# Kernel optimization log

Hardware: AMD Instinct MI355X
Metric: run time of the kernel (lower is better)

Reference implementation:

```python
import jax, jax.numpy as jnp
import numpy as np

EPS = 1e-6

def elu_feature_map(x):
    return jax.nn.elu(x) + 1.0

def setup_inputs() -> dict:
    key = jax.random.key(0)
    k1, k2, k3 = jax.random.split(key, 3)
    N, S, H, D, M = 16, 4096, 16, 64, 64
    query = jax.random.normal(k1, (N, H, D), dtype=jnp.float32)
    keys = jax.random.normal(k2, (N, S, H, D), dtype=jnp.float32)
    values = jax.random.normal(k3, (N, S, H, M), dtype=jnp.float32)
    key_mask = jnp.ones((N, S), dtype=jnp.float32)  # key_lengths.float_matrix
    return {"query": query, "keys": keys, "values": values, "key_mask": key_mask}

def reference(query, keys, values, key_mask):
    # Q: [N,H,D]
    Q = elu_feature_map(query)
    # K: [N,S,H,D], masked over sequence
    K = elu_feature_map(keys) * key_mask[:, :, None, None]
    # S_state: [N,H,M,D] -- K^T V outer-product reduction over sequence
    S_state = jnp.einsum('nshd,nshm->nhmd', K, values)
    # Z: [N,H,D] -- normalizer
    Z = K.sum(axis=1)
    # QZ: [N,H]
    QZ = 1.0 / (jnp.einsum('nhd,nhd->nh', Q, Z) + EPS)
    # V_out: [N,H,M]
    V_out = jnp.einsum('nhd,nhmd,nh->nhm', Q, S_state, QZ)
    return (V_out, S_state, Z)
```

## Files before the change

### kernel.cpp

```cpp
#include <hip/hip_runtime.h>


#define S_LEN  4096
#define NHEAD  16
#define DDIM   64
#define MDIM   64
#define NWAVE  4
#define CH_S   32
#define PITCH  1024
#define WS_ROW 4160

#define OUT_SOFF  (16 * 16 * 64)
#define OUT_ZOFF  (OUT_SOFF + 16 * 16 * 64 * 64)

using short8 = __attribute__((ext_vector_type(8))) short;
using f32x4  = __attribute__((ext_vector_type(4))) float;
using uint4v = __attribute__((ext_vector_type(4))) unsigned int;

union FragCast { uint4v u; short8 s; };

__device__ __forceinline__ float elup1(float x) {
    return x > 0.0f ? x + 1.0f : __expf(x);
}

__device__ __forceinline__ unsigned bfpack(float a, float b) {
    union { float f; unsigned u; } ca, cb;
    ca.f = a; cb.f = b;
    const unsigned ra = ca.u + 0x7FFFu + ((ca.u >> 16) & 1u);
    const unsigned rb = cb.u + 0x7FFFu + ((cb.u >> 16) & 1u);
    return (ra >> 16) | (rb & 0xFFFF0000u);
}

__device__ __forceinline__ const float* rfl_ptr(const float* p) {
    unsigned long long u = (unsigned long long)p;
    const unsigned lo = __builtin_amdgcn_readfirstlane((unsigned)u);
    const unsigned hi = __builtin_amdgcn_readfirstlane((unsigned)(u >> 32));
    return (const float*)(((unsigned long long)hi << 32) | lo);
}

__global__ __launch_bounds__(256, 1)
void rcla_partial(const float* __restrict__ keys,
                  const float* __restrict__ values,
                  const float* __restrict__ kmask,
                  float* __restrict__ ws,
                  int nchk, int psh)
{
    __shared__ float mbuf[64][68];

    const int t    = threadIdx.x;
    const int wave = t >> 6;
    const int lane = t & 63;
    const int c16  = lane & 15;
    const int g    = lane >> 4;
    const int part = blockIdx.x & ((1 << psh) - 1);
    const int pair = blockIdx.x >> psh;
    const int nIdx = pair >> 4;
    const int hIdx = pair & 15;

    const int sWave = part * (S_LEN >> psh) + wave * (nchk * CH_S);
    const size_t base = ((size_t)nIdx * S_LEN + sWave) * PITCH
                      + (size_t)hIdx * DDIM;
    const float* kbase = rfl_ptr(keys   + base) ;
    const float* vbase = rfl_ptr(values + base);
    const float* mbase = rfl_ptr(kmask + (size_t)nIdx * S_LEN + sWave);

    f32x4 acc[4][4];
#pragma unroll
    for (int i = 0; i < 4; ++i)
#pragma unroll
        for (int j = 0; j < 4; ++j) acc[i][j] = f32x4{0.f, 0.f, 0.f, 0.f};
    float zz[4] = {0.f, 0.f, 0.f, 0.f};

    for (int ch = 0; ch < nchk; ++ch) {
        const int s0 = ch * CH_S + g * 8;

        float kraw[4][8];
#pragma unroll
        for (int j = 0; j < 8; ++j) {
            const size_t ro = (size_t)(s0 + j) * PITCH + c16;
#pragma unroll
            for (int tj = 0; tj < 4; ++tj)
                kraw[tj][j] = kbase[ro + tj * 16];
        }
        float mk[8];
#pragma unroll
        for (int j = 0; j < 8; ++j) mk[j] = mbase[s0 + j];

        float vraw[4][8];
#pragma unroll
        for (int j = 0; j < 8; ++j) {
            const size_t ro = (size_t)(s0 + j) * PITCH + c16;
#pragma unroll
            for (int ti = 0; ti < 4; ++ti)
                vraw[ti][j] = vbase[ro + ti * 16];
        }

        unsigned kf[4][4], vf[4][4];
#pragma unroll
        for (int tj = 0; tj < 4; ++tj)
#pragma unroll
            for (int q = 0; q < 4; ++q) {
                const float e0 = elup1(kraw[tj][2 * q])     * mk[2 * q];
                const float e1 = elup1(kraw[tj][2 * q + 1]) * mk[2 * q + 1];
                zz[tj] += e0 + e1;
                kf[tj][q] = bfpack(e0, e1);
            }
#pragma unroll
        for (int ti = 0; ti < 4; ++ti)
#pragma unroll
            for (int q = 0; q < 4; ++q)
                vf[ti][q] = bfpack(vraw[ti][2 * q], vraw[ti][2 * q + 1]);

#pragma unroll
        for (int ti = 0; ti < 4; ++ti) {
            FragCast fa;
            fa.u = uint4v{vf[ti][0], vf[ti][1], vf[ti][2], vf[ti][3]};
#pragma unroll
            for (int tj = 0; tj < 4; ++tj) {
                FragCast fb;
                fb.u = uint4v{kf[tj][0], kf[tj][1], kf[tj][2], kf[tj][3]};
                acc[ti][tj] = __builtin_amdgcn_mfma_f32_16x16x32_bf16(
                    fa.s, fb.s, acc[ti][tj], 0, 0, 0);
            }
        }
    }

#pragma unroll
    for (int tj = 0; tj < 4; ++tj) {
        zz[tj] += __shfl_xor(zz[tj], 16, 64);
        zz[tj] += __shfl_xor(zz[tj], 32, 64);
    }

    __syncthreads();

    for (int rr = 0; rr < 4; ++rr) {
        if (wave == rr) {
#pragma unroll
            for (int ti = 0; ti < 4; ++ti)
#pragma unroll
                for (int tj = 0; tj < 4; ++tj)
#pragma unroll
                    for (int r = 0; r < 4; ++r) {
                        const int m = ti * 16 + g * 4 + r;
                        const int d = tj * 16 + c16;
                        if (rr == 0) mbuf[m][d]  = acc[ti][tj][r];
                        else         mbuf[m][d] += acc[ti][tj][r];
                    }
        }
        __syncthreads();
    }

    float* wrow = ws + (size_t)blockIdx.x * WS_ROW;
    {
        const int m  = t >> 2;
        const int dc = (t & 3) * 16;
#pragma unroll
        for (int j = 0; j < 16; j += 4)
            *(float4*)&wrow[m * 64 + dc + j] = *(const float4*)&mbuf[m][dc + j];
    }
    __syncthreads();

    if (g == 0) {
#pragma unroll
        for (int tj = 0; tj < 4; ++tj)
            mbuf[wave][tj * 16 + c16] = zz[tj];
    }
    __syncthreads();
    if (t < 64) {
        float zv = 0.f;
#pragma unroll
        for (int r = 0; r < NWAVE; ++r) zv += mbuf[r][t];
        wrow[64 * 64 + t] = zv;
    }
}

__global__ __launch_bounds__(256)
void rcla_reduce(const float* __restrict__ query,
                 const float* __restrict__ ws,
                 float* __restrict__ out,
                 int nsplit)
{
    __shared__ float S[64][68];
    __shared__ float zb[64];
    __shared__ float qb[64];

    const int p = blockIdx.x;
    const int t = threadIdx.x;
    const float* bp = ws + (size_t)p * nsplit * WS_ROW;

    const int m  = t >> 2;
    const int dc = (t & 3) * 16;
    float4 a[4];
#pragma unroll
    for (int j = 0; j < 4; ++j) a[j] = make_float4(0.f, 0.f, 0.f, 0.f);
    for (int part = 0; part < nsplit; ++part) {
        const float* w = bp + (size_t)part * WS_ROW + m * 64 + dc;
#pragma unroll
        for (int j = 0; j < 4; ++j) {
            const float4 x = *(const float4*)&w[j * 4];
            a[j].x += x.x; a[j].y += x.y; a[j].z += x.z; a[j].w += x.w;
        }
    }
#pragma unroll
    for (int j = 0; j < 4; ++j) {
        *(float4*)&out[OUT_SOFF + (size_t)p * 4096 + m * 64 + dc + j * 4] = a[j];
        *(float4*)&S[m][dc + j * 4] = a[j];
    }
    if (t < 64) {
        float zv = 0.f;
        for (int part = 0; part < nsplit; ++part)
            zv += bp[(size_t)part * WS_ROW + 64 * 64 + t];
        out[OUT_ZOFF + (size_t)p * 64 + t] = zv;
        zb[t] = zv;
        qb[t] = elup1(query[(size_t)p * 64 + t]);
    }
    __syncthreads();

    if (t < 64) {
        float zp = qb[t] * zb[t];
#pragma unroll
        for (int off = 32; off >= 1; off >>= 1) zp += __shfl_xor(zp, off, 64);
        const float qz = 1.0f / (zp + 1e-6f);
        float vs = 0.0f;
#pragma unroll
        for (int d = 0; d < 64; d += 4) {
            const float4 sv = *(const float4*)&S[t][d];
            vs = fmaf(qb[d],     sv.x, vs);
            vs = fmaf(qb[d + 1], sv.y, vs);
            vs = fmaf(qb[d + 2], sv.z, vs);
            vs = fmaf(qb[d + 3], sv.w, vs);
        }
        out[(size_t)p * 64 + t] = qz * vs;
    }
}

extern "C" void kernel_launch(void* const* d_in, const int* in_sizes, int n_in,
                              void* d_out, int out_size, void* d_ws, size_t ws_size,
                              hipStream_t stream) {
    const float* q  = (const float*)d_in[0];
    const float* k  = (const float*)d_in[1];
    const float* v  = (const float*)d_in[2];
    const float* km = (const float*)d_in[3];
    float* out = (float*)d_out;
    float* wsf = (float*)d_ws;

    int psh = 2;
    if (ws_size < (size_t)256 * 4 * WS_ROW * sizeof(float)) psh = 1;
    if (ws_size < (size_t)256 * 2 * WS_ROW * sizeof(float)) psh = 0;
    const int split = 1 << psh;
    const int nchk  = (S_LEN >> psh) / (NWAVE * CH_S);

    rcla_partial<<<dim3(256 * split), dim3(256), 0, stream>>>(k, v, km, wsf, nchk, psh);
    rcla_reduce <<<dim3(256),         dim3(256), 0, stream>>>(q, wsf, out, split);
}
```

Baseline: 124.1 us.

## Fuse partial and reduce kernels with double-buffered global-to-LDS async loads

Merges the split partial kernel and the reduce kernel into one kernel with one block per (n,h) pair, which removes the workspace round trip and the second launch. Keys, values and mask are streamed into a per-wave double-buffered LDS area with global_load_lds, gated by vmcnt waits, so memory fetch overlaps the MFMA compute of the previous chunk. The trade-off is only 256 blocks of 4 waves each and no sequence split, so there may be too little parallelism to saturate HBM on a 256-CU part. Correctness relies on the hand-counted vmcnt values matching the 17 loads issued per chunk.

```diff
diff --git a/kernel.cpp b/kernel.cpp
--- a/kernel.cpp
+++ b/kernel.cpp
@@ -7,8 +7,8 @@
 #define MDIM   64
 #define NWAVE  4
 #define CH_S   32
+#define NCHK   32
 #define PITCH  1024
-#define WS_ROW 4160
 
 #define OUT_SOFF  (16 * 16 * 64)
 #define OUT_ZOFF  (OUT_SOFF + 16 * 16 * 64 * 64)
@@ -18,6 +18,18 @@
 using uint4v = __attribute__((ext_vector_type(4))) unsigned int;
 
 union FragCast { uint4v u; short8 s; };
+
+typedef const __attribute__((address_space(1))) void gvoid_t;
+typedef __attribute__((address_space(3))) void lvoid_t;
+
+#define GLOAD16(dst, src) \
+    __builtin_amdgcn_global_load_lds((gvoid_t*)(src), (lvoid_t*)(dst), 16, 0, 0)
+#define GLOAD4(dst, src) \
+    __builtin_amdgcn_global_load_lds((gvoid_t*)(src), (lvoid_t*)(dst), 4, 0, 0)
+#define WAITVM17 do { asm volatile("s_waitcnt vmcnt(17)" ::: "memory"); \
+                      __builtin_amdgcn_sched_barrier(0); } while (0)
+#define WAITVM0  do { asm volatile("s_waitcnt vmcnt(0)"  ::: "memory"); \
+                      __builtin_amdgcn_sched_barrier(0); } while (0)
 
 __device__ __forceinline__ float elup1(float x) {
     return x > 0.0f ? x + 1.0f : __expf(x);
@@ -31,38 +43,42 @@
     return (ra >> 16) | (rb & 0xFFFF0000u);
 }
 
-__device__ __forceinline__ const float* rfl_ptr(const float* p) {
-    unsigned long long u = (unsigned long long)p;
-    const unsigned lo = __builtin_amdgcn_readfirstlane((unsigned)u);
-    const unsigned hi = __builtin_amdgcn_readfirstlane((unsigned)(u >> 32));
-    return (const float*)(((unsigned long long)hi << 32) | lo);
-}
+struct WaveBuf {
+    float K[CH_S][DDIM];
+    float V[CH_S][MDIM];
+    float mk[64];
+};
 
 __global__ __launch_bounds__(256, 1)
-void rcla_partial(const float* __restrict__ keys,
-                  const float* __restrict__ values,
-                  const float* __restrict__ kmask,
-                  float* __restrict__ ws,
-                  int nchk, int psh)
+void rcla_fused(const float* __restrict__ query,
+                const float* __restrict__ keys,
+                const float* __restrict__ values,
+                const float* __restrict__ kmask,
+                float* __restrict__ out)
 {
+    __shared__ WaveBuf hot[NWAVE][2];
     __shared__ float mbuf[64][68];
+    __shared__ float zrows[NWAVE][64];
+    __shared__ float qb[64];
+    __shared__ float zb[64];
 
     const int t    = threadIdx.x;
     const int wave = t >> 6;
     const int lane = t & 63;
     const int c16  = lane & 15;
     const int g    = lane >> 4;
-    const int part = blockIdx.x & ((1 << psh) - 1);
-    const int pair = blockIdx.x >> psh;
+    const int pair = blockIdx.x;
     const int nIdx = pair >> 4;
     const int hIdx = pair & 15;
 
-    const int sWave = part * (S_LEN >> psh) + wave * (nchk * CH_S);
+    const int sWave = wave * (NCHK * CH_S);
     const size_t base = ((size_t)nIdx * S_LEN + sWave) * PITCH
                       + (size_t)hIdx * DDIM;
-    const float* kbase = rfl_ptr(keys   + base) ;
-    const float* vbase = rfl_ptr(values + base);
-    const float* mbase = rfl_ptr(kmask + (size_t)nIdx * S_LEN + sWave);
+    const int li = lane >> 4;
+    const int ci = lane & 15;
+    const float* kl = keys   + base + (size_t)li * PITCH + ci * 4;
+    const float* vl = values + base + (size_t)li * PITCH + ci * 4;
+    const float* ml = kmask + (size_t)nIdx * S_LEN + sWave + (lane & 31);
 
     f32x4 acc[4][4];
 #pragma unroll
@@ -71,37 +87,43 @@
         for (int j = 0; j < 4; ++j) acc[i][j] = f32x4{0.f, 0.f, 0.f, 0.f};
     float zz[4] = {0.f, 0.f, 0.f, 0.f};
 
-    for (int ch = 0; ch < nchk; ++ch) {
-        const int s0 = ch * CH_S + g * 8;
-
-        float kraw[4][8];
-#pragma unroll
-        for (int j = 0; j < 8; ++j) {
-            const size_t ro = (size_t)(s0 + j) * PITCH + c16;
-#pragma unroll
-            for (int tj = 0; tj < 4; ++tj)
-                kraw[tj][j] = kbase[ro + tj * 16];
-        }
-        float mk[8];
-#pragma unroll
-        for (int j = 0; j < 8; ++j) mk[j] = mbase[s0 + j];
-
-        float vraw[4][8];
-#pragma unroll
-        for (int j = 0; j < 8; ++j) {
-            const size_t ro = (size_t)(s0 + j) * PITCH + c16;
-#pragma unroll
-            for (int ti = 0; ti < 4; ++ti)
-                vraw[ti][j] = vbase[ro + ti * 16];
-        }
+    auto issue = [&](int p, int ch) {
+        const size_t co = (size_t)ch * CH_S * PITCH;
+        float* Kd = &hot[wave][p].K[0][0];
+        float* Vd = &hot[wave][p].V[0][0];
+#pragma unroll
+        for (int r = 0; r < 8; ++r)
+            GLOAD16(Kd + r * 256, kl + co + (size_t)r * 4 * PITCH);
+#pragma unroll
+        for (int r = 0; r < 8; ++r)
+            GLOAD16(Vd + r * 256, vl + co + (size_t)r * 4 * PITCH);
+        GLOAD4(&hot[wave][p].mk[0], ml + ch * CH_S);
+    };
+
+    auto compute = [&](int p) {
+        const WaveBuf& B = hot[wave][p];
+        float mk8[8];
+#pragma unroll
+        for (int j = 0; j < 8; ++j) mk8[j] = B.mk[g * 8 + j];
+        float kraw[4][8], vraw[4][8];
+#pragma unroll
+        for (int tj = 0; tj < 4; ++tj)
+#pragma unroll
+            for (int j = 0; j < 8; ++j)
+                kraw[tj][j] = B.K[g * 8 + j][tj * 16 + c16];
+#pragma unroll
+        for (int ti = 0; ti < 4; ++ti)
+#pragma unroll
+            for (int j = 0; j < 8; ++j)
+                vraw[ti][j] = B.V[g * 8 + j][ti * 16 + c16];
 
         unsigned kf[4][4], vf[4][4];
 #pragma unroll
         for (int tj = 0; tj < 4; ++tj)
 #pragma unroll
             for (int q = 0; q < 4; ++q) {
-                const float e0 = elup1(kraw[tj][2 * q])     * mk[2 * q];
-                const float e1 = elup1(kraw[tj][2 * q + 1]) * mk[2 * q + 1];
+                const float e0 = elup1(kraw[tj][2 * q])     * mk8[2 * q];
+                const float e1 = elup1(kraw[tj][2 * q + 1]) * mk8[2 * q + 1];
                 zz[tj] += e0 + e1;
                 kf[tj][q] = bfpack(e0, e1);
             }
@@ -123,7 +145,23 @@
                     fa.s, fb.s, acc[ti][tj], 0, 0, 0);
             }
         }
-    }
+    };
+
+    issue(0, 0);
+#pragma unroll 1
+    for (int c = 0; c < NCHK - 2; c += 2) {
+        issue(1, c + 1);
+        WAITVM17;
+        compute(0);
+        issue(0, c + 2);
+        WAITVM17;
+        compute(1);
+    }
+    issue(1, NCHK - 1);
+    WAITVM17;
+    compute(0);
+    WAITVM0;
+    compute(1);
 
 #pragma unroll
     for (int tj = 0; tj < 4; ++tj) {
@@ -150,87 +188,45 @@
         __syncthreads();
     }
 
-    float* wrow = ws + (size_t)blockIdx.x * WS_ROW;
+    if (g == 0) {
+#pragma unroll
+        for (int tj = 0; tj < 4; ++tj)
+            zrows[wave][tj * 16 + c16] = zz[tj];
+    }
+    if (t < 64) qb[t] = elup1(query[(size_t)pair * DDIM + t]);
+
     {
         const int m  = t >> 2;
         const int dc = (t & 3) * 16;
 #pragma unroll
         for (int j = 0; j < 16; j += 4)
-            *(float4*)&wrow[m * 64 + dc + j] = *(const float4*)&mbuf[m][dc + j];
+            *(float4*)&out[OUT_SOFF + (size_t)pair * 4096 + m * 64 + dc + j] =
+                *(const float4*)&mbuf[m][dc + j];
     }
     __syncthreads();
 
-    if (g == 0) {
-#pragma unroll
-        for (int tj = 0; tj < 4; ++tj)
-            mbuf[wave][tj * 16 + c16] = zz[tj];
+    if (t < 64) {
+        const float zv = zrows[0][t] + zrows[1][t] + zrows[2][t] + zrows[3][t];
+        out[OUT_ZOFF + (size_t)pair * 64 + t] = zv;
+        zb[t] = zv;
     }
     __syncthreads();
-    if (t < 64) {
-        float zv = 0.f;
-#pragma unroll
-        for (int r = 0; r < NWAVE; ++r) zv += mbuf[r][t];
-        wrow[64 * 64 + t] = zv;
-    }
-}
-
-__global__ __launch_bounds__(256)
-void rcla_reduce(const float* __restrict__ query,
-                 const float* __restrict__ ws,
-                 float* __restrict__ out,
-                 int nsplit)
-{
-    __shared__ float S[64][68];
-    __shared__ float zb[64];
-    __shared__ float qb[64];
-
-    const int p = blockIdx.x;
-    const int t = threadIdx.x;
-    const float* bp = ws + (size_t)p * nsplit * WS_ROW;
-
-    const int m  = t >> 2;
-    const int dc = (t & 3) * 16;
-    float4 a[4];
-#pragma unroll
-    for (int j = 0; j < 4; ++j) a[j] = make_float4(0.f, 0.f, 0.f, 0.f);
-    for (int part = 0; part < nsplit; ++part) {
-        const float* w = bp + (size_t)part * WS_ROW + m * 64 + dc;
-#pragma unroll
-        for (int j = 0; j < 4; ++j) {
-            const float4 x = *(const float4*)&w[j * 4];
-            a[j].x += x.x; a[j].y += x.y; a[j].z += x.z; a[j].w += x.w;
-        }
-    }
-#pragma unroll
-    for (int j = 0; j < 4; ++j) {
-        *(float4*)&out[OUT_SOFF + (size_t)p * 4096 + m * 64 + dc + j * 4] = a[j];
-        *(float4*)&S[m][dc + j * 4] = a[j];
-    }
-    if (t < 64) {
-        float zv = 0.f;
-        for (int part = 0; part < nsplit; ++part)
-            zv += bp[(size_t)part * WS_ROW + 64 * 64 + t];
-        out[OUT_ZOFF + (size_t)p * 64 + t] = zv;
-        zb[t] = zv;
-        qb[t] = elup1(query[(size_t)p * 64 + t]);
-    }
-    __syncthreads();
-
-    if (t < 64) {
-        float zp = qb[t] * zb[t];
+
+    if (wave == 0) {
+        float zp = qb[lane] * zb[lane];
 #pragma unroll
         for (int off = 32; off >= 1; off >>= 1) zp += __shfl_xor(zp, off, 64);
         const float qz = 1.0f / (zp + 1e-6f);
         float vs = 0.0f;
 #pragma unroll
         for (int d = 0; d < 64; d += 4) {
-            const float4 sv = *(const float4*)&S[t][d];
+            const float4 sv = *(const float4*)&mbuf[lane][d];
             vs = fmaf(qb[d],     sv.x, vs);
             vs = fmaf(qb[d + 1], sv.y, vs);
             vs = fmaf(qb[d + 2], sv.z, vs);
             vs = fmaf(qb[d + 3], sv.w, vs);
         }
-        out[(size_t)p * 64 + t] = qz * vs;
+        out[(size_t)pair * MDIM + lane] = qz * vs;
     }
 }
 
@@ -242,14 +238,5 @@
     const float* v  = (const float*)d_in[2];
     const float* km = (const float*)d_in[3];
     float* out = (float*)d_out;
-    float* wsf = (float*)d_ws;
-
-    int psh = 2;
-    if (ws_size < (size_t)256 * 4 * WS_ROW * sizeof(float)) psh = 1;
-    if (ws_size < (size_t)256 * 2 * WS_ROW * sizeof(float)) psh = 0;
-    const int split = 1 << psh;
-    const int nchk  = (S_LEN >> psh) / (NWAVE * CH_S);
-
-    rcla_partial<<<dim3(256 * split), dim3(256), 0, stream>>>(k, v, km, wsf, nchk, psh);
-    rcla_reduce <<<dim3(256),         dim3(256), 0, stream>>>(q, wsf, out, split);
-}
+    rcla_fused<<<dim3(256), dim3(256), 0, stream>>>(q, k, v, km, out);
+}
```

Measured after the change: 106.3 us. -14.4%, faster.

## Stream K/V through LDS via async global_load_lds with 4-stage per-wave pipeline

Applied to the files above, without the earlier changes.

Replaces direct per-lane global loads of keys and values with asynchronous global_load_lds copies into a 4-deep per-wave LDS ring, using explicit vmcnt waits so loads for upcoming chunks overlap with transform and MFMA work on the current one. The split across sequence parts is removed: each block now covers one (n,h) pair and each wave writes its own partial S and Z row straight to workspace, which the reduce kernel sums, dropping the LDS cross-wave reduction and its barriers. Half the lanes transform each 16-row chunk alternately, and MFMAs fire every two chunks. The grid shrinks to 256 blocks with large LDS use, which may lower occupancy and memory-level parallelism, and the fixed workspace size no longer falls back when ws_size is small.

```diff
diff --git a/kernel.cpp b/kernel.cpp
--- a/kernel.cpp
+++ b/kernel.cpp
@@ -6,7 +6,8 @@
 #define DDIM   64
 #define MDIM   64
 #define NWAVE  4
-#define CH_S   32
+#define CH_S   16
+#define NCHK   64
 #define PITCH  1024
 #define WS_ROW 4160
 
@@ -18,6 +19,16 @@
 using uint4v = __attribute__((ext_vector_type(4))) unsigned int;
 
 union FragCast { uint4v u; short8 s; };
+
+typedef const __attribute__((address_space(1))) void gvoid_t;
+typedef __attribute__((address_space(3))) void lvoid_t;
+
+#define GLOAD16(dst, src) \
+    __builtin_amdgcn_global_load_lds((gvoid_t*)(src), (lvoid_t*)(dst), 16, 0, 0)
+#define GLOAD4(dst, src) \
+    __builtin_amdgcn_global_load_lds((gvoid_t*)(src), (lvoid_t*)(dst), 4, 0, 0)
+#define WAITVM(N) do { asm volatile("s_waitcnt vmcnt(" #N ")" ::: "memory"); \
+                       __builtin_amdgcn_sched_barrier(0); } while (0)
 
 __device__ __forceinline__ float elup1(float x) {
     return x > 0.0f ? x + 1.0f : __expf(x);
@@ -31,38 +42,34 @@
     return (ra >> 16) | (rb & 0xFFFF0000u);
 }
 
-__device__ __forceinline__ const float* rfl_ptr(const float* p) {
-    unsigned long long u = (unsigned long long)p;
-    const unsigned lo = __builtin_amdgcn_readfirstlane((unsigned)u);
-    const unsigned hi = __builtin_amdgcn_readfirstlane((unsigned)(u >> 32));
-    return (const float*)(((unsigned long long)hi << 32) | lo);
-}
-
 __global__ __launch_bounds__(256, 1)
 void rcla_partial(const float* __restrict__ keys,
                   const float* __restrict__ values,
                   const float* __restrict__ kmask,
-                  float* __restrict__ ws,
-                  int nchk, int psh)
+                  float* __restrict__ ws)
 {
-    __shared__ float mbuf[64][68];
+    __shared__ float Kbuf[NWAVE][4][CH_S * DDIM];
+    __shared__ float Vbuf[NWAVE][4][CH_S * DDIM];
+    __shared__ float maskL[NWAVE][1024];
 
     const int t    = threadIdx.x;
     const int wave = t >> 6;
     const int lane = t & 63;
     const int c16  = lane & 15;
     const int g    = lane >> 4;
-    const int part = blockIdx.x & ((1 << psh) - 1);
-    const int pair = blockIdx.x >> psh;
+    const int pair = blockIdx.x;
     const int nIdx = pair >> 4;
     const int hIdx = pair & 15;
 
-    const int sWave = part * (S_LEN >> psh) + wave * (nchk * CH_S);
+    const int sWave = wave * (NCHK * CH_S);
     const size_t base = ((size_t)nIdx * S_LEN + sWave) * PITCH
                       + (size_t)hIdx * DDIM;
-    const float* kbase = rfl_ptr(keys   + base) ;
-    const float* vbase = rfl_ptr(values + base);
-    const float* mbase = rfl_ptr(kmask + (size_t)nIdx * S_LEN + sWave);
+    const int li = lane >> 4;
+    const int ci = lane & 15;
+    const float* kl = keys   + base + (size_t)li * PITCH + ci * 4;
+    const float* vl = values + base + (size_t)li * PITCH + ci * 4;
+    const float* msrc = kmask + (size_t)nIdx * S_LEN + sWave + lane;
+    float* maskb = &maskL[wave][0];
 
     f32x4 acc[4][4];
 #pragma unroll
@@ -70,47 +77,56 @@
 #pragma unroll
         for (int j = 0; j < 4; ++j) acc[i][j] = f32x4{0.f, 0.f, 0.f, 0.f};
     float zz[4] = {0.f, 0.f, 0.f, 0.f};
-
-    for (int ch = 0; ch < nchk; ++ch) {
-        const int s0 = ch * CH_S + g * 8;
-
-        float kraw[4][8];
-#pragma unroll
-        for (int j = 0; j < 8; ++j) {
-            const size_t ro = (size_t)(s0 + j) * PITCH + c16;
+    unsigned kf[4][4], vf[4][4];
+
+    auto issue = [&](int b, int ch) {
+        const size_t co = (size_t)ch * CH_S * PITCH;
+        float* Kd = &Kbuf[wave][0][0] + b * (CH_S * DDIM);
+        float* Vd = &Vbuf[wave][0][0] + b * (CH_S * DDIM);
+#pragma unroll
+        for (int r = 0; r < 4; ++r)
+            GLOAD16(Kd + r * 256, kl + co + (size_t)r * 4 * PITCH);
+#pragma unroll
+        for (int r = 0; r < 4; ++r)
+            GLOAD16(Vd + r * 256, vl + co + (size_t)r * 4 * PITCH);
+    };
+
+    auto xform = [&](int b, int ch, int par) {
+        if ((g >> 1) == par) {
+            const int r0 = (g & 1) * 8;
+            const float* Kb = &Kbuf[wave][0][0] + b * (CH_S * DDIM);
+            const float* Vb = &Vbuf[wave][0][0] + b * (CH_S * DDIM);
+            float mk8[8], kraw[4][8], vraw[4][8];
+#pragma unroll
+            for (int j = 0; j < 8; ++j) mk8[j] = maskb[ch * CH_S + r0 + j];
 #pragma unroll
             for (int tj = 0; tj < 4; ++tj)
-                kraw[tj][j] = kbase[ro + tj * 16];
-        }
-        float mk[8];
-#pragma unroll
-        for (int j = 0; j < 8; ++j) mk[j] = mbase[s0 + j];
-
-        float vraw[4][8];
-#pragma unroll
-        for (int j = 0; j < 8; ++j) {
-            const size_t ro = (size_t)(s0 + j) * PITCH + c16;
+#pragma unroll
+                for (int j = 0; j < 8; ++j)
+                    kraw[tj][j] = Kb[(r0 + j) * DDIM + tj * 16 + c16];
 #pragma unroll
             for (int ti = 0; ti < 4; ++ti)
-                vraw[ti][j] = vbase[ro + ti * 16];
-        }
-
-        unsigned kf[4][4], vf[4][4];
-#pragma unroll
-        for (int tj = 0; tj < 4; ++tj)
-#pragma unroll
-            for (int q = 0; q < 4; ++q) {
-                const float e0 = elup1(kraw[tj][2 * q])     * mk[2 * q];
-                const float e1 = elup1(kraw[tj][2 * q + 1]) * mk[2 * q + 1];
-                zz[tj] += e0 + e1;
-                kf[tj][q] = bfpack(e0, e1);
-            }
-#pragma unroll
-        for (int ti = 0; ti < 4; ++ti)
-#pragma unroll
-            for (int q = 0; q < 4; ++q)
-                vf[ti][q] = bfpack(vraw[ti][2 * q], vraw[ti][2 * q + 1]);
-
+#pragma unroll
+                for (int j = 0; j < 8; ++j)
+                    vraw[ti][j] = Vb[(r0 + j) * DDIM + ti * 16 + c16];
+#pragma unroll
+            for (int tj = 0; tj < 4; ++tj)
+#pragma unroll
+                for (int q = 0; q < 4; ++q) {
+                    const float e0 = elup1(kraw[tj][2 * q])     * mk8[2 * q];
+                    const float e1 = elup1(kraw[tj][2 * q + 1]) * mk8[2 * q + 1];
+                    zz[tj] += e0 + e1;
+                    kf[tj][q] = bfpack(e0, e1);
+                }
+#pragma unroll
+            for (int ti = 0; ti < 4; ++ti)
+#pragma unroll
+                for (int q = 0; q < 4; ++q)
+                    vf[ti][q] = bfpack(vraw[ti][2 * q], vraw[ti][2 * q + 1]);
+        }
+    };
+
+    auto domfma = [&]() {
 #pragma unroll
         for (int ti = 0; ti < 4; ++ti) {
             FragCast fa;
@@ -123,7 +139,27 @@
                     fa.s, fb.s, acc[ti][tj], 0, 0, 0);
             }
         }
-    }
+    };
+
+#pragma unroll
+    for (int grp = 0; grp < 16; ++grp)
+        GLOAD4(maskb + grp * 64, msrc + grp * 64);
+    issue(0, 0);
+    issue(1, 1);
+    issue(2, 2);
+
+#pragma unroll 1
+    for (int tt = 0; tt < 15; ++tt) {
+        const int c0 = 4 * tt;
+        WAITVM(16); issue(3, c0 + 3); xform(0, c0 + 0, 0);
+        WAITVM(16); issue(0, c0 + 4); xform(1, c0 + 1, 1); domfma();
+        WAITVM(16); issue(1, c0 + 5); xform(2, c0 + 2, 0);
+        WAITVM(16); issue(2, c0 + 6); xform(3, c0 + 3, 1); domfma();
+    }
+    WAITVM(16); issue(3, 63); xform(0, 60, 0);
+    WAITVM(16);               xform(1, 61, 1); domfma();
+    WAITVM(8);                xform(2, 62, 0);
+    WAITVM(0);                xform(3, 63, 1); domfma();
 
 #pragma unroll
     for (int tj = 0; tj < 4; ++tj) {
@@ -131,46 +167,18 @@
         zz[tj] += __shfl_xor(zz[tj], 32, 64);
     }
 
-    __syncthreads();
-
-    for (int rr = 0; rr < 4; ++rr) {
-        if (wave == rr) {
-#pragma unroll
-            for (int ti = 0; ti < 4; ++ti)
-#pragma unroll
-                for (int tj = 0; tj < 4; ++tj)
-#pragma unroll
-                    for (int r = 0; r < 4; ++r) {
-                        const int m = ti * 16 + g * 4 + r;
-                        const int d = tj * 16 + c16;
-                        if (rr == 0) mbuf[m][d]  = acc[ti][tj][r];
-                        else         mbuf[m][d] += acc[ti][tj][r];
-                    }
-        }
-        __syncthreads();
-    }
-
-    float* wrow = ws + (size_t)blockIdx.x * WS_ROW;
-    {
-        const int m  = t >> 2;
-        const int dc = (t & 3) * 16;
-#pragma unroll
-        for (int j = 0; j < 16; j += 4)
-            *(float4*)&wrow[m * 64 + dc + j] = *(const float4*)&mbuf[m][dc + j];
-    }
-    __syncthreads();
-
+    float* wrow = ws + ((size_t)pair * NWAVE + wave) * WS_ROW;
+#pragma unroll
+    for (int ti = 0; ti < 4; ++ti)
+#pragma unroll
+        for (int tj = 0; tj < 4; ++tj)
+#pragma unroll
+            for (int r = 0; r < 4; ++r)
+                wrow[(ti * 16 + g * 4 + r) * 64 + tj * 16 + c16] = acc[ti][tj][r];
     if (g == 0) {
 #pragma unroll
         for (int tj = 0; tj < 4; ++tj)
-            mbuf[wave][tj * 16 + c16] = zz[tj];
-    }
-    __syncthreads();
-    if (t < 64) {
-        float zv = 0.f;
-#pragma unroll
-        for (int r = 0; r < NWAVE; ++r) zv += mbuf[r][t];
-        wrow[64 * 64 + t] = zv;
+            wrow[64 * 64 + tj * 16 + c16] = zz[tj];
     }
 }
 
@@ -244,12 +252,6 @@
     float* out = (float*)d_out;
     float* wsf = (float*)d_ws;
 
-    int psh = 2;
-    if (ws_size < (size_t)256 * 4 * WS_ROW * sizeof(float)) psh = 1;
-    if (ws_size < (size_t)256 * 2 * WS_ROW * sizeof(float)) psh = 0;
-    const int split = 1 << psh;
-    const int nchk  = (S_LEN >> psh) / (NWAVE * CH_S);
-
-    rcla_partial<<<dim3(256 * split), dim3(256), 0, stream>>>(k, v, km, wsf, nchk, psh);
-    rcla_reduce <<<dim3(256),         dim3(256), 0, stream>>>(q, wsf, out, split);
-}
+    rcla_partial<<<dim3(256), dim3(256), 0, stream>>>(k, v, km, wsf);
+    rcla_reduce <<<dim3(256), dim3(256), 0, stream>>>(q, wsf, out, NWAVE);
+}
```

New measurement: 143.9 us. 15.9% more time.
